# Kernel optimization log

Measured on AMD Instinct MI355X. Metric: run time of the kernel, lower is better.

The kernel has to match this reference:

```python
import jax, jax.numpy as jnp
import numpy as np

S, B, D = 2048, 2, 1024   # seq_len, batch, d_model
H, Dh = 16, 64            # n_head, d_head (H*Dh == D)
LN_EPS = 1e-5


def _rel_shift(x):
    # x: [qlen, klen, bsz, n_head] -- standard Transformer-XL relative shift
    q, k, b, n = x.shape
    x = jnp.pad(x, ((0, 0), (1, 0), (0, 0), (0, 0)))  # [q, k+1, b, n]
    x = x.reshape(k + 1, q, b, n)[1:]                  # drop first row
    return x.reshape(q, k, b, n)


def setup_inputs() -> dict:
    key = jax.random.key(0)
    ks = jax.random.split(key, 8)
    s = 0.02
    return {
        "x":    jax.random.normal(ks[0], (S, B, D), jnp.float32),
        "r":    jax.random.normal(ks[1], (1, D), jnp.float32),          # learned pos vector
        "rw":   jax.random.normal(ks[2], (H, Dh), jnp.float32),          # content bias
        "rr":   jax.random.normal(ks[3], (H, Dh), jnp.float32),          # position bias
        "ln_g": jnp.ones((D,), jnp.float32),
        "ln_b": jnp.zeros((D,), jnp.float32),
        "Wqkv": jax.random.normal(ks[4], (D, 3 * H * Dh), jnp.float32) * s,
        "Wr":   jax.random.normal(ks[5], (D, H * Dh), jnp.float32) * s,
        "Wo":   jax.random.normal(ks[6], (H * Dh, D), jnp.float32) * s,
    }


def reference(x, r, rw, rr, ln_g, ln_b, Wqkv, Wr, Wo):
    # Pre-LayerNorm (dropout = identity in eval mode)
    mu = jnp.mean(x, axis=-1, keepdims=True)
    var = jnp.mean(jnp.square(x - mu), axis=-1, keepdims=True)
    xn = (x - mu) * jax.lax.rsqrt(var + LN_EPS) * ln_g + ln_b   # [S,B,D]

    # relative position input: r expanded over seq
    r_exp = jnp.broadcast_to(r, (S, D))                          # [S,D]

    qkv = xn @ Wqkv                                              # [S,B,3*H*Dh]
    q, k, v = jnp.split(qkv, 3, axis=-1)
    q = q.reshape(S, B, H, Dh)
    k = k.reshape(S, B, H, Dh)
    v = v.reshape(S, B, H, Dh)
    rk = (r_exp @ Wr).reshape(S, H, Dh)                          # [S,H,Dh]

    scale = 1.0 / np.sqrt(Dh).astype(np.float32)
    AC = jnp.einsum('ibnd,jbnd->ijbn', q + rw, k)                # content term
    BD = jnp.einsum('ibnd,jnd->ijbn', q + rr, rk)                # position term
    BD = _rel_shift(BD)
    attn = jax.nn.softmax((AC + BD) * scale, axis=1)             # over key axis j

    av = jnp.einsum('ijbn,jbnd->ibnd', attn, v).reshape(S, B, H * Dh)
    return xn + av @ Wo                                          # residual w/ normed input
```

## Files before the change

kernel.cpp:

```cpp
#include <hip/hip_runtime.h>

typedef unsigned short u16;
typedef __attribute__((ext_vector_type(8))) __bf16 bf16x8;
typedef __attribute__((ext_vector_type(8))) u16 u16x8;
typedef __attribute__((ext_vector_type(4))) float f32x4;

__device__ __forceinline__ float bf2f(u16 u){
  union { unsigned int i; float f; } v; v.i = ((unsigned int)u) << 16; return v.f;
}
__device__ __forceinline__ u16 f2bf(float f){
  union { float f; unsigned int u; } v; v.f = f;
  unsigned int u = v.u;
  u += 0x7FFFu + ((u >> 16) & 1u);
  return (u16)(u >> 16);
}
__device__ __forceinline__ void gld_lds16(const u16* g, u16* l){
  __builtin_amdgcn_global_load_lds((const __attribute__((address_space(1))) unsigned int*)g,
                                   (__attribute__((address_space(3))) unsigned int*)l, 16, 0, 0);
}

__global__ __launch_bounds__(256) void transpose_k(const float* __restrict__ in, u16* __restrict__ out,
                                                   int R, int C){
  __shared__ float tile[32][33];
  const int bx = blockIdx.x * 32, by = blockIdx.y * 32;
  const int tx = threadIdx.x, ty = threadIdx.y;
  #pragma unroll
  for(int i = 0; i < 32; i += 8)
    tile[ty + i][tx] = in[(size_t)(by + ty + i) * C + bx + tx];
  __syncthreads();
  #pragma unroll
  for(int i = 0; i < 32; i += 8)
    out[(size_t)(bx + ty + i) * R + by + tx] = f2bf(tile[tx][ty + i]);
}

__global__ __launch_bounds__(256) void ln_k(const float* __restrict__ x, const float* __restrict__ gw,
                                            const float* __restrict__ bw, u16* __restrict__ xnb){
  const int row = blockIdx.x, t = threadIdx.x;
  const float* xr = x + (size_t)row * 1024;
  float4 xv = *reinterpret_cast<const float4*>(xr + t * 4);
  float s  = xv.x + xv.y + xv.z + xv.w;
  float s2 = xv.x*xv.x + xv.y*xv.y + xv.z*xv.z + xv.w*xv.w;
  #pragma unroll
  for(int m = 1; m <= 32; m <<= 1){ s += __shfl_xor(s, m, 64); s2 += __shfl_xor(s2, m, 64); }
  __shared__ float red[8];
  const int w = t >> 6, lane = t & 63;
  if(lane == 0){ red[w] = s; red[4 + w] = s2; }
  __syncthreads();
  float S1 = red[0] + red[1] + red[2] + red[3];
  float S2 = red[4] + red[5] + red[6] + red[7];
  float mu = S1 * (1.f/1024.f);
  float var = S2 * (1.f/1024.f) - mu * mu;
  float rstd = rsqrtf(var + 1e-5f);
  float4 gv = *reinterpret_cast<const float4*>(gw + t * 4);
  float4 bv = *reinterpret_cast<const float4*>(bw + t * 4);
  ushort4 o;
  o.x = f2bf((xv.x - mu) * rstd * gv.x + bv.x);
  o.y = f2bf((xv.y - mu) * rstd * gv.y + bv.y);
  o.z = f2bf((xv.z - mu) * rstd * gv.z + bv.z);
  o.w = f2bf((xv.w - mu) * rstd * gv.w + bv.w);
  *reinterpret_cast<ushort4*>(xnb + (size_t)row * 1024 + t * 4) = o;
}

__global__ __launch_bounds__(256) void rk0_k(const float* __restrict__ r, const float* __restrict__ Wr,
                                             float* __restrict__ rk0){
  const int n = blockIdx.x * 256 + threadIdx.x;
  const int d0 = blockIdx.y * 128;
  float acc = 0.f;
  for(int d = d0; d < d0 + 128; ++d)
    acc += r[d] * Wr[(size_t)d * 1024 + n];
  atomicAdd(&rk0[n], acc);
}

__global__ __launch_bounds__(256) void c_k(const u16* __restrict__ qk, const float* __restrict__ rr,
                                           const float* __restrict__ rk0, float* __restrict__ cc){
  const int w = threadIdx.x >> 6, lane = threadIdx.x & 63;
  const int ib = blockIdx.x * 4 + w;
  const u16* qp = qk + (size_t)ib * 2048 + lane * 16;
  u16x8 q0 = *reinterpret_cast<const u16x8*>(qp);
  u16x8 q1 = *reinterpret_cast<const u16x8*>(qp + 8);
  const float* rrp = rr + lane * 16;
  const float* rkp = rk0 + lane * 16;
  float s = 0.f;
  #pragma unroll
  for(int e = 0; e < 8; ++e){
    s += (bf2f(q0[e]) + rrp[e]) * rkp[e];
    s += (bf2f(q1[e]) + rrp[8 + e]) * rkp[8 + e];
  }
  s += __shfl_xor(s, 1, 64);
  s += __shfl_xor(s, 2, 64);
  if((lane & 3) == 0) cc[(size_t)ib * 16 + (lane >> 2)] = s;
}

template<int MODE>
__global__ __launch_bounds__(256) void gemm_bt_k(const u16* __restrict__ A, const u16* __restrict__ BT,
                                                 const u16* __restrict__ res, u16* __restrict__ Cb,
                                                 float* __restrict__ Cf, u16* __restrict__ vT,
                                                 int M, int N, int K){
  __shared__ u16 sA[128 * 32];
  __shared__ u16 sB[128 * 32];
  const int t = threadIdx.x;
  const int row0 = blockIdx.y * 128, col0 = blockIdx.x * 128;
  const int w = t >> 6, lane = t & 63, g = lane >> 4, lq = lane & 15;
  const int wr = (w >> 1) * 64, wc = (w & 1) * 64;
  const int s0 = t, s1 = t + 256;
  f32x4 zero4 = {0.f, 0.f, 0.f, 0.f};
  f32x4 acc[4][4];
  #pragma unroll
  for(int mi = 0; mi < 4; ++mi)
    #pragma unroll
    for(int ni = 0; ni < 4; ++ni) acc[mi][ni] = zero4;

  for(int kt = 0; kt < K; kt += 32){
    gld_lds16(A  + (size_t)(row0 + (s0 >> 2)) * K + kt + (s0 & 3) * 8, &sA[w * 512]);
    gld_lds16(A  + (size_t)(row0 + (s1 >> 2)) * K + kt + (s1 & 3) * 8, &sA[2048 + w * 512]);
    gld_lds16(BT + (size_t)(col0 + (s0 >> 2)) * K + kt + (s0 & 3) * 8, &sB[w * 512]);
    gld_lds16(BT + (size_t)(col0 + (s1 >> 2)) * K + kt + (s1 & 3) * 8, &sB[2048 + w * 512]);
    __syncthreads();
    bf16x8 af[4];
    #pragma unroll
    for(int mi = 0; mi < 4; ++mi)
      af[mi] = *reinterpret_cast<const bf16x8*>(&sA[(wr + mi * 16 + lq) * 32 + g * 8]);
    #pragma unroll
    for(int ni = 0; ni < 4; ++ni){
      bf16x8 bfr = *reinterpret_cast<const bf16x8*>(&sB[(wc + ni * 16 + lq) * 32 + g * 8]);
      #pragma unroll
      for(int mi = 0; mi < 4; ++mi)
        acc[mi][ni] = __builtin_amdgcn_mfma_f32_16x16x32_bf16(af[mi], bfr, acc[mi][ni], 0, 0, 0);
    }
    __syncthreads();
  }
  #pragma unroll
  for(int mi = 0; mi < 4; ++mi)
    #pragma unroll
    for(int ni = 0; ni < 4; ++ni)
      #pragma unroll
      for(int rg = 0; rg < 4; ++rg){
        const int row = row0 + wr + mi * 16 + g * 4 + rg;
        const int col = col0 + wc + ni * 16 + lq;
        float v = acc[mi][ni][rg];
        if(MODE == 1){
          v += bf2f(res[(size_t)row * N + col]);
          Cf[(size_t)row * N + col] = v;
        } else {
          if(col < 2048){
            Cb[(size_t)row * 2048 + col] = f2bf(v);
          } else {
            const int b = row & 1, i = row >> 1, h = (col - 2048) >> 6, d = col & 63;
            vT[((size_t)((b << 4) + h) * 64 + d) * 2048 + i] = f2bf(v);
          }
        }
      }
}

__global__ __launch_bounds__(256) void attn_k(const u16* __restrict__ qk, const u16* __restrict__ vT,
                                              const float* __restrict__ rw, const float* __restrict__ cc,
                                              u16* __restrict__ av){
  constexpr int S = 2048;
  __shared__ u16 ks[2][64 * 72];
  __shared__ u16 vs[2][64 * 72];
  __shared__ u16 ps[4][16 * 72];
  const int t = threadIdx.x;
  const int i0 = blockIdx.x * 64;
  const int bh = blockIdx.y;
  const int b = bh >> 4, h = bh & 15;
  const int w = t >> 6, lane = t & 63, g = lane >> 4, lq = lane & 15;
  const float scale = 0.125f;

  bf16x8 aq0, aq1;
  {
    const int irow = (i0 + w * 16 + lq) * 2 + b;
    const u16* qp = qk + (size_t)irow * 2048 + h * 64;
    u16x8 q0 = *reinterpret_cast<const u16x8*>(qp + g * 8);
    u16x8 q1 = *reinterpret_cast<const u16x8*>(qp + 32 + g * 8);
    const float* rwp = rw + h * 64 + g * 8;
    u16x8 a0, a1;
    #pragma unroll
    for(int e = 0; e < 8; ++e){
      a0[e] = f2bf((bf2f(q0[e]) + rwp[e]) * scale);
      a1[e] = f2bf((bf2f(q1[e]) + rwp[32 + e]) * scale);
    }
    aq0 = *reinterpret_cast<bf16x8*>(&a0);
    aq1 = *reinterpret_cast<bf16x8*>(&a1);
  }
  float ci[4], cp[4];
  #pragma unroll
  for(int rg = 0; rg < 4; ++rg){
    const int i = i0 + w * 16 + g * 4 + rg;
    ci[rg] = cc[(size_t)(i * 2 + b) * 16 + h] * scale;
    cp[rg] = (i + 1 < S) ? cc[(size_t)((i + 1) * 2 + b) * 16 + h] * scale : 0.0f;
  }
  float rsum[4] = {0.f, 0.f, 0.f, 0.f};
  f32x4 zero4 = {0.f, 0.f, 0.f, 0.f};
  f32x4 acc[4];
  #pragma unroll
  for(int ni = 0; ni < 4; ++ni) acc[ni] = zero4;

  const int jr = t >> 2, c0 = (t & 3) * 16;
  {
    const u16* kp = qk + (size_t)(jr * 2 + b) * 2048 + 1024 + h * 64 + c0;
    *reinterpret_cast<u16x8*>(&ks[0][jr * 72 + c0])     = *reinterpret_cast<const u16x8*>(kp);
    *reinterpret_cast<u16x8*>(&ks[0][jr * 72 + c0 + 8]) = *reinterpret_cast<const u16x8*>(kp + 8);
    const u16* vp = vT + ((size_t)bh * 64 + jr) * 2048 + c0;
    *reinterpret_cast<u16x8*>(&vs[0][jr * 72 + c0])     = *reinterpret_cast<const u16x8*>(vp);
    *reinterpret_cast<u16x8*>(&vs[0][jr * 72 + c0 + 8]) = *reinterpret_cast<const u16x8*>(vp + 8);
  }
  __syncthreads();

  for(int n = 0; n < 32; ++n){
    const int p = n & 1;
    u16x8 k0, k1, v0, v1;
    const bool pre = (n + 1 < 32);
    if(pre){
      const int j0n = (n + 1) * 64;
      const u16* kp = qk + (size_t)((j0n + jr) * 2 + b) * 2048 + 1024 + h * 64 + c0;
      k0 = *reinterpret_cast<const u16x8*>(kp);
      k1 = *reinterpret_cast<const u16x8*>(kp + 8);
      const u16* vp = vT + ((size_t)bh * 64 + jr) * 2048 + j0n + c0;
      v0 = *reinterpret_cast<const u16x8*>(vp);
      v1 = *reinterpret_cast<const u16x8*>(vp + 8);
    }
    const int j0 = n * 64;
    #pragma unroll
    for(int jt = 0; jt < 4; ++jt){
      f32x4 s4 = zero4;
      bf16x8 b0 = *reinterpret_cast<const bf16x8*>(&ks[p][(jt * 16 + lq) * 72 + g * 8]);
      s4 = __builtin_amdgcn_mfma_f32_16x16x32_bf16(aq0, b0, s4, 0, 0, 0);
      bf16x8 b1 = *reinterpret_cast<const bf16x8*>(&ks[p][(jt * 16 + lq) * 72 + 32 + g * 8]);
      s4 = __builtin_amdgcn_mfma_f32_16x16x32_bf16(aq1, b1, s4, 0, 0, 0);
      const int j = j0 + jt * 16 + lq;
      #pragma unroll
      for(int rg = 0; rg < 4; ++rg){
        const int i = i0 + w * 16 + g * 4 + rg;
        const float t1 = (j <= i) ? ci[rg] : cp[rg];
        const float bd = (j == i + 1) ? 0.0f : t1;
        const float pv = __expf(s4[rg] + bd);
        rsum[rg] += pv;
        ps[w][(g * 4 + rg) * 72 + jt * 16 + lq] = f2bf(pv);
      }
    }
    __asm__ __volatile__("s_waitcnt lgkmcnt(0)" ::: "memory");
    bf16x8 ap0 = *reinterpret_cast<const bf16x8*>(&ps[w][lq * 72 + g * 8]);
    bf16x8 ap1 = *reinterpret_cast<const bf16x8*>(&ps[w][lq * 72 + 32 + g * 8]);
    #pragma unroll
    for(int ni = 0; ni < 4; ++ni){
      bf16x8 bv0 = *reinterpret_cast<const bf16x8*>(&vs[p][(ni * 16 + lq) * 72 + g * 8]);
      acc[ni] = __builtin_amdgcn_mfma_f32_16x16x32_bf16(ap0, bv0, acc[ni], 0, 0, 0);
      bf16x8 bv1 = *reinterpret_cast<const bf16x8*>(&vs[p][(ni * 16 + lq) * 72 + 32 + g * 8]);
      acc[ni] = __builtin_amdgcn_mfma_f32_16x16x32_bf16(ap1, bv1, acc[ni], 0, 0, 0);
    }
    if(pre){
      const int q2 = p ^ 1;
      *reinterpret_cast<u16x8*>(&ks[q2][jr * 72 + c0])     = k0;
      *reinterpret_cast<u16x8*>(&ks[q2][jr * 72 + c0 + 8]) = k1;
      *reinterpret_cast<u16x8*>(&vs[q2][jr * 72 + c0])     = v0;
      *reinterpret_cast<u16x8*>(&vs[q2][jr * 72 + c0 + 8]) = v1;
    }
    __syncthreads();
  }
  #pragma unroll
  for(int rg = 0; rg < 4; ++rg){
    #pragma unroll
    for(int m = 1; m <= 8; m <<= 1) rsum[rg] += __shfl_xor(rsum[rg], m, 64);
    rsum[rg] = 1.0f / rsum[rg];
  }
  #pragma unroll
  for(int ni = 0; ni < 4; ++ni)
    #pragma unroll
    for(int rg = 0; rg < 4; ++rg){
      const int i = i0 + w * 16 + g * 4 + rg;
      const int d = ni * 16 + lq;
      av[(size_t)(i * 2 + b) * 1024 + h * 64 + d] = f2bf(acc[ni][rg] * rsum[rg]);
    }
}

extern "C" void kernel_launch(void* const* d_in, const int* in_sizes, int n_in,
                              void* d_out, int out_size, void* d_ws, size_t ws_size,
                              hipStream_t stream){
  (void)in_sizes; (void)n_in; (void)out_size; (void)ws_size;
  const float* x    = (const float*)d_in[0];
  const float* r    = (const float*)d_in[1];
  const float* rw   = (const float*)d_in[2];
  const float* rr   = (const float*)d_in[3];
  const float* ln_g = (const float*)d_in[4];
  const float* ln_b = (const float*)d_in[5];
  const float* Wqkv = (const float*)d_in[6];
  const float* Wr   = (const float*)d_in[7];
  const float* Wo   = (const float*)d_in[8];
  char* ws = (char*)d_ws;
  u16*   xnb   = (u16*)(ws + 0);
  u16*   qk    = (u16*)(ws + 8388608);
  u16*   av    = (u16*)(ws + 25165824);
  u16*   woT   = (u16*)(ws + 33554432);
  u16*   wqkvT = (u16*)(ws + 35651584);
  u16*   vT    = (u16*)(ws + 41943040);
  float* rk0   = (float*)(ws + 50331648);
  float* cc    = (float*)(ws + 50335744);
  float* out   = (float*)d_out;

  transpose_k<<<dim3(96, 32), dim3(32, 8), 0, stream>>>(Wqkv, wqkvT, 1024, 3072);
  transpose_k<<<dim3(32, 32), dim3(32, 8), 0, stream>>>(Wo, woT, 1024, 1024);
  ln_k<<<4096, 256, 0, stream>>>(x, ln_g, ln_b, xnb);
  hipMemsetAsync(rk0, 0, 4096, stream);
  rk0_k<<<dim3(4, 8), 256, 0, stream>>>(r, Wr, rk0);
  gemm_bt_k<2><<<dim3(24, 32), 256, 0, stream>>>(xnb, wqkvT, nullptr, qk, nullptr, vT, 4096, 3072, 1024);
  c_k<<<1024, 256, 0, stream>>>(qk, rr, rk0, cc);
  attn_k<<<dim3(32, 32), 256, 0, stream>>>(qk, vT, rw, cc, av);
  gemm_bt_k<1><<<dim3(8, 32), 256, 0, stream>>>(av, woT, xnb, nullptr, out, nullptr, 4096, 1024, 1024);
}
```

Baseline: 264.0 us.

## Swap MFMA operands in attention, compute row sums via MFMA, separate V transpose

The QKV GEMM now writes V in natural layout and a new tiled LDS transpose kernel builds vT, replacing scattered 2-byte strided global stores in the GEMM epilogue. In attention, MFMA operands are swapped so each lane owns one query row, which allows branch-free exp2 for tiles fully below or above the diagonal. Probabilities are packed into bf16 pairs with perm, and row sums come from an extra MFMA against a ones vector instead of shuffles. The change adds one kernel launch and an extra pass over V, and the sum is now taken from the bf16-rounded probabilities.

```diff
diff --git a/kernel.cpp b/kernel.cpp
--- a/kernel.cpp
+++ b/kernel.cpp
@@ -13,6 +13,9 @@
   unsigned int u = v.u;
   u += 0x7FFFu + ((u >> 16) & 1u);
   return (u16)(u >> 16);
+}
+__device__ __forceinline__ unsigned fbits(float f){
+  union { float f; unsigned u; } v; v.f = f; return v.u;
 }
 __device__ __forceinline__ void gld_lds16(const u16* g, u16* l){
   __builtin_amdgcn_global_load_lds((const __attribute__((address_space(1))) unsigned int*)g,
@@ -91,10 +94,31 @@
   if((lane & 3) == 0) cc[(size_t)ib * 16 + (lane >> 2)] = s;
 }
 
+__global__ __launch_bounds__(256) void vtrans_k(const u16* __restrict__ vnat, u16* __restrict__ vT){
+  __shared__ u16 tl[128][40];
+  const int t = threadIdx.x;
+  const int i0 = blockIdx.x * 128, c0 = blockIdx.y * 32, b = blockIdx.z;
+  {
+    const int ii = t & 127, cs = (t >> 7) * 16;
+    const u16* p = vnat + (size_t)((i0 + ii) * 2 + b) * 1024 + c0 + cs;
+    *reinterpret_cast<u16x8*>(&tl[ii][cs])     = *reinterpret_cast<const u16x8*>(p);
+    *reinterpret_cast<u16x8*>(&tl[ii][cs + 8]) = *reinterpret_cast<const u16x8*>(p + 8);
+  }
+  __syncthreads();
+  const int dr = t & 31, seg = t >> 5;
+  const int R = (b * 16 + (c0 >> 6)) * 64 + (c0 & 63) + dr;
+  u16 tmp[16];
+  #pragma unroll
+  for(int e = 0; e < 16; ++e) tmp[e] = tl[seg * 16 + e][dr];
+  u16* op = vT + (size_t)R * 2048 + i0 + seg * 16;
+  *reinterpret_cast<u16x8*>(op)     = *reinterpret_cast<u16x8*>(&tmp[0]);
+  *reinterpret_cast<u16x8*>(op + 8) = *reinterpret_cast<u16x8*>(&tmp[8]);
+}
+
 template<int MODE>
 __global__ __launch_bounds__(256) void gemm_bt_k(const u16* __restrict__ A, const u16* __restrict__ BT,
                                                  const u16* __restrict__ res, u16* __restrict__ Cb,
-                                                 float* __restrict__ Cf, u16* __restrict__ vT,
+                                                 float* __restrict__ Cf, u16* __restrict__ vnat,
                                                  int M, int N, int K){
   __shared__ u16 sA[128 * 32];
   __shared__ u16 sB[128 * 32];
@@ -142,12 +166,8 @@
           v += bf2f(res[(size_t)row * N + col]);
           Cf[(size_t)row * N + col] = v;
         } else {
-          if(col < 2048){
-            Cb[(size_t)row * 2048 + col] = f2bf(v);
-          } else {
-            const int b = row & 1, i = row >> 1, h = (col - 2048) >> 6, d = col & 63;
-            vT[((size_t)((b << 4) + h) * 64 + d) * 2048 + i] = f2bf(v);
-          }
+          if(col < 2048) Cb[(size_t)row * 2048 + col] = f2bf(v);
+          else           vnat[(size_t)row * 1024 + (col - 2048)] = f2bf(v);
         }
       }
 }
@@ -164,12 +184,14 @@
   const int bh = blockIdx.y;
   const int b = bh >> 4, h = bh & 15;
   const int w = t >> 6, lane = t & 63, g = lane >> 4, lq = lane & 15;
+  const int iw0 = i0 + w * 16;
+  const int i_lane = iw0 + lq;
   const float scale = 0.125f;
+  const float L2E = 1.4426950408889634f;
 
   bf16x8 aq0, aq1;
   {
-    const int irow = (i0 + w * 16 + lq) * 2 + b;
-    const u16* qp = qk + (size_t)irow * 2048 + h * 64;
+    const u16* qp = qk + (size_t)(i_lane * 2 + b) * 2048 + h * 64;
     u16x8 q0 = *reinterpret_cast<const u16x8*>(qp + g * 8);
     u16x8 q1 = *reinterpret_cast<const u16x8*>(qp + 32 + g * 8);
     const float* rwp = rw + h * 64 + g * 8;
@@ -182,18 +204,20 @@
     aq0 = *reinterpret_cast<bf16x8*>(&a0);
     aq1 = *reinterpret_cast<bf16x8*>(&a1);
   }
-  float ci[4], cp[4];
-  #pragma unroll
-  for(int rg = 0; rg < 4; ++rg){
-    const int i = i0 + w * 16 + g * 4 + rg;
-    ci[rg] = cc[(size_t)(i * 2 + b) * 16 + h] * scale;
-    cp[rg] = (i + 1 < S) ? cc[(size_t)((i + 1) * 2 + b) * 16 + h] * scale : 0.0f;
-  }
-  float rsum[4] = {0.f, 0.f, 0.f, 0.f};
+  const float ciL = cc[(size_t)(i_lane * 2 + b) * 16 + h] * scale * L2E;
+  const float cpL = (i_lane + 1 < S) ? cc[(size_t)((i_lane + 1) * 2 + b) * 16 + h] * scale * L2E : 0.0f;
+
   f32x4 zero4 = {0.f, 0.f, 0.f, 0.f};
-  f32x4 acc[4];
+  f32x4 acc[4], acc5 = zero4;
   #pragma unroll
   for(int ni = 0; ni < 4; ++ni) acc[ni] = zero4;
+  bf16x8 ones;
+  {
+    u16x8 ob;
+    #pragma unroll
+    for(int e = 0; e < 8; ++e) ob[e] = 0x3F80;
+    ones = *reinterpret_cast<bf16x8*>(&ob);
+  }
 
   const int jr = t >> 2, c0 = (t & 3) * 16;
   {
@@ -220,23 +244,37 @@
       v1 = *reinterpret_cast<const u16x8*>(vp + 8);
     }
     const int j0 = n * 64;
+    const bool below = (j0 + 63 <= iw0);
+    const bool above = (j0 >= iw0 + 17);
     #pragma unroll
     for(int jt = 0; jt < 4; ++jt){
       f32x4 s4 = zero4;
       bf16x8 b0 = *reinterpret_cast<const bf16x8*>(&ks[p][(jt * 16 + lq) * 72 + g * 8]);
-      s4 = __builtin_amdgcn_mfma_f32_16x16x32_bf16(aq0, b0, s4, 0, 0, 0);
+      s4 = __builtin_amdgcn_mfma_f32_16x16x32_bf16(b0, aq0, s4, 0, 0, 0);
       bf16x8 b1 = *reinterpret_cast<const bf16x8*>(&ks[p][(jt * 16 + lq) * 72 + 32 + g * 8]);
-      s4 = __builtin_amdgcn_mfma_f32_16x16x32_bf16(aq1, b1, s4, 0, 0, 0);
-      const int j = j0 + jt * 16 + lq;
-      #pragma unroll
-      for(int rg = 0; rg < 4; ++rg){
-        const int i = i0 + w * 16 + g * 4 + rg;
-        const float t1 = (j <= i) ? ci[rg] : cp[rg];
-        const float bd = (j == i + 1) ? 0.0f : t1;
-        const float pv = __expf(s4[rg] + bd);
-        rsum[rg] += pv;
-        ps[w][(g * 4 + rg) * 72 + jt * 16 + lq] = f2bf(pv);
+      s4 = __builtin_amdgcn_mfma_f32_16x16x32_bf16(b1, aq1, s4, 0, 0, 0);
+      float pv[4];
+      if(below){
+        #pragma unroll
+        for(int rg = 0; rg < 4; ++rg)
+          pv[rg] = __builtin_amdgcn_exp2f(fmaf(s4[rg], L2E, ciL));
+      } else if(above){
+        #pragma unroll
+        for(int rg = 0; rg < 4; ++rg)
+          pv[rg] = __builtin_amdgcn_exp2f(fmaf(s4[rg], L2E, cpL));
+      } else {
+        #pragma unroll
+        for(int rg = 0; rg < 4; ++rg){
+          const int j = j0 + jt * 16 + g * 4 + rg;
+          const float t1 = (j <= i_lane) ? ciL : cpL;
+          const float bdL = (j == i_lane + 1) ? 0.0f : t1;
+          pv[rg] = __builtin_amdgcn_exp2f(fmaf(s4[rg], L2E, bdL));
+        }
       }
+      uint2 pk;
+      pk.x = __builtin_amdgcn_perm(fbits(pv[1]), fbits(pv[0]), 0x07060302);
+      pk.y = __builtin_amdgcn_perm(fbits(pv[3]), fbits(pv[2]), 0x07060302);
+      *reinterpret_cast<uint2*>(&ps[w][lq * 72 + jt * 16 + g * 4]) = pk;
     }
     __asm__ __volatile__("s_waitcnt lgkmcnt(0)" ::: "memory");
     bf16x8 ap0 = *reinterpret_cast<const bf16x8*>(&ps[w][lq * 72 + g * 8]);
@@ -244,10 +282,12 @@
     #pragma unroll
     for(int ni = 0; ni < 4; ++ni){
       bf16x8 bv0 = *reinterpret_cast<const bf16x8*>(&vs[p][(ni * 16 + lq) * 72 + g * 8]);
-      acc[ni] = __builtin_amdgcn_mfma_f32_16x16x32_bf16(ap0, bv0, acc[ni], 0, 0, 0);
+      acc[ni] = __builtin_amdgcn_mfma_f32_16x16x32_bf16(bv0, ap0, acc[ni], 0, 0, 0);
       bf16x8 bv1 = *reinterpret_cast<const bf16x8*>(&vs[p][(ni * 16 + lq) * 72 + 32 + g * 8]);
-      acc[ni] = __builtin_amdgcn_mfma_f32_16x16x32_bf16(ap1, bv1, acc[ni], 0, 0, 0);
-    }
+      acc[ni] = __builtin_amdgcn_mfma_f32_16x16x32_bf16(bv1, ap1, acc[ni], 0, 0, 0);
+    }
+    acc5 = __builtin_amdgcn_mfma_f32_16x16x32_bf16(ones, ap0, acc5, 0, 0, 0);
+    acc5 = __builtin_amdgcn_mfma_f32_16x16x32_bf16(ones, ap1, acc5, 0, 0, 0);
     if(pre){
       const int q2 = p ^ 1;
       *reinterpret_cast<u16x8*>(&ks[q2][jr * 72 + c0])     = k0;
@@ -257,20 +297,17 @@
     }
     __syncthreads();
   }
-  #pragma unroll
-  for(int rg = 0; rg < 4; ++rg){
-    #pragma unroll
-    for(int m = 1; m <= 8; m <<= 1) rsum[rg] += __shfl_xor(rsum[rg], m, 64);
-    rsum[rg] = 1.0f / rsum[rg];
-  }
-  #pragma unroll
-  for(int ni = 0; ni < 4; ++ni)
-    #pragma unroll
-    for(int rg = 0; rg < 4; ++rg){
-      const int i = i0 + w * 16 + g * 4 + rg;
-      const int d = ni * 16 + lq;
-      av[(size_t)(i * 2 + b) * 1024 + h * 64 + d] = f2bf(acc[ni][rg] * rsum[rg]);
-    }
+  const float rinv = 1.0f / acc5[0];
+  #pragma unroll
+  for(int ni = 0; ni < 4; ++ni){
+    ushort4 o;
+    o.x = f2bf(acc[ni][0] * rinv);
+    o.y = f2bf(acc[ni][1] * rinv);
+    o.z = f2bf(acc[ni][2] * rinv);
+    o.w = f2bf(acc[ni][3] * rinv);
+    const int d = ni * 16 + g * 4;
+    *reinterpret_cast<ushort4*>(av + (size_t)(i_lane * 2 + b) * 1024 + h * 64 + d) = o;
+  }
 }
 
 extern "C" void kernel_launch(void* const* d_in, const int* in_sizes, int n_in,
@@ -295,6 +332,7 @@
   u16*   vT    = (u16*)(ws + 41943040);
   float* rk0   = (float*)(ws + 50331648);
   float* cc    = (float*)(ws + 50335744);
+  u16*   vnat  = av;
   float* out   = (float*)d_out;
 
   transpose_k<<<dim3(96, 32), dim3(32, 8), 0, stream>>>(Wqkv, wqkvT, 1024, 3072);
@@ -302,7 +340,8 @@
   ln_k<<<4096, 256, 0, stream>>>(x, ln_g, ln_b, xnb);
   hipMemsetAsync(rk0, 0, 4096, stream);
   rk0_k<<<dim3(4, 8), 256, 0, stream>>>(r, Wr, rk0);
-  gemm_bt_k<2><<<dim3(24, 32), 256, 0, stream>>>(xnb, wqkvT, nullptr, qk, nullptr, vT, 4096, 3072, 1024);
+  gemm_bt_k<2><<<dim3(24, 32), 256, 0, stream>>>(xnb, wqkvT, nullptr, qk, nullptr, vnat, 4096, 3072, 1024);
+  vtrans_k<<<dim3(16, 32, 2), 256, 0, stream>>>(vnat, vT);
   c_k<<<1024, 256, 0, stream>>>(qk, rr, rk0, cc);
   attn_k<<<dim3(32, 32), 256, 0, stream>>>(qk, vT, rw, cc, av);
   gemm_bt_k<1><<<dim3(8, 32), 256, 0, stream>>>(av, woT, xnb, nullptr, out, nullptr, 4096, 1024, 1024);
```

Result: faster. 253.9 us (-3.8%).
